# Performance work log

Hardware: AMD Instinct MI355X
Metric: run time of the kernel (lower is better)

The kernel has to match this reference:

```python
import jax, jax.numpy as jnp
from jax import lax
import numpy as np

PRE_NMS_TOPN = 2000
POST_NMS_TOPN = 300
NMS_IOU_THRESHOLD = 0.7
EPS = 1e-8


def setup_inputs() -> dict:
    key = jax.random.key(0)
    k1, k2 = jax.random.split(key, 2)
    B, H, W, A = 64, 100, 100, 9
    # small-magnitude deltas so exp(dh/dw) stays sane, as real RPN outputs do
    rpn_bbox_deltas = jax.random.normal(k1, (B, H, W, A * 4), dtype=jnp.float32) * 0.1
    rpn_labels = jax.random.uniform(k2, (B, H, W, A), dtype=jnp.float32)
    # grid anchors, normalized coords, 3 scales x 3 ratios = 9 per position
    ys = (jnp.arange(H, dtype=jnp.float32) + 0.5) / H
    xs = (jnp.arange(W, dtype=jnp.float32) + 0.5) / W
    scales = jnp.array([0.1, 0.2, 0.4], dtype=jnp.float32)
    ratios = jnp.array([0.5, 1.0, 2.0], dtype=jnp.float32)
    hh = (scales[:, None] * jnp.sqrt(ratios)[None, :]).reshape(-1)  # [9]
    ww = (scales[:, None] / jnp.sqrt(ratios)[None, :]).reshape(-1)  # [9]
    cy, cx = jnp.meshgrid(ys, xs, indexing="ij")  # [H,W]
    cy, cx = cy[..., None], cx[..., None]         # [H,W,1]
    anchors = jnp.stack(
        [cy - hh / 2, cx - ww / 2, cy + hh / 2, cx + ww / 2], axis=-1
    ).reshape(-1, 4)  # [H*W*9, 4] = [90000, 4]
    return {"rpn_bbox_deltas": rpn_bbox_deltas, "rpn_labels": rpn_labels, "anchors": anchors}


def _decode_deltas(anchors, deltas):
    # anchors [N,4] (y1,x1,y2,x2), deltas [B,N,4] (dy,dx,dh,dw)
    anc_h = anchors[:, 2] - anchors[:, 0]
    anc_w = anchors[:, 3] - anchors[:, 1]
    anc_cy = anchors[:, 0] + 0.5 * anc_h
    anc_cx = anchors[:, 1] + 0.5 * anc_w
    h = jnp.exp(deltas[..., 2]) * anc_h
    w = jnp.exp(deltas[..., 3]) * anc_w
    cy = deltas[..., 0] * anc_h + anc_cy
    cx = deltas[..., 1] * anc_w + anc_cx
    y1 = cy - 0.5 * h
    x1 = cx - 0.5 * w
    return jnp.stack([y1, x1, y1 + h, x1 + w], axis=-1)  # [B,N,4]


def _nms_single(boxes):
    # boxes [PRE,4] already sorted by score descending; greedy hard NMS
    n = boxes.shape[0]
    area = jnp.maximum(boxes[:, 2] - boxes[:, 0], 0.0) * jnp.maximum(boxes[:, 3] - boxes[:, 1], 0.0)
    idx = jnp.arange(n)

    def body(i, keep):
        b = boxes[i]
        yy1 = jnp.maximum(b[0], boxes[:, 0])
        xx1 = jnp.maximum(b[1], boxes[:, 1])
        yy2 = jnp.minimum(b[2], boxes[:, 2])
        xx2 = jnp.minimum(b[3], boxes[:, 3])
        inter = jnp.maximum(yy2 - yy1, 0.0) * jnp.maximum(xx2 - xx1, 0.0)
        iou = inter / (area[i] + area - inter + EPS)
        suppress = (iou > NMS_IOU_THRESHOLD) & (idx > i) & keep[i]
        return keep & ~suppress

    keep = lax.fori_loop(0, n, body, jnp.ones((n,), dtype=bool))
    # compact kept boxes (score order) into fixed [POST,4], zero-padded
    pos = jnp.where(keep, jnp.cumsum(keep) - 1, POST_NMS_TOPN)
    pos = jnp.minimum(pos, POST_NMS_TOPN)
    out = jnp.zeros((POST_NMS_TOPN + 1, 4), dtype=boxes.dtype).at[pos].set(boxes)[:POST_NMS_TOPN]
    return jnp.clip(out, 0.0, 1.0)  # clip_boxes=True in tf combined NMS


def reference(rpn_bbox_deltas, rpn_labels, anchors):
    B = rpn_bbox_deltas.shape[0]
    N = anchors.shape[0]
    deltas = rpn_bbox_deltas.reshape(B, N, 4)
    labels = rpn_labels.reshape(B, N)
    boxes = _decode_deltas(anchors, deltas)             # [B,N,4]
    _, pre_idx = lax.top_k(labels, PRE_NMS_TOPN)        # [B,PRE] sorted desc
    pre_boxes = jnp.take_along_axis(boxes, pre_idx[..., None], axis=1)  # [B,PRE,4]
    roi_bboxes = jax.vmap(_nms_single)(pre_boxes)       # [B,POST,4]
    return lax.stop_gradient(roi_bboxes)
```

## Files before the change

kernel.cpp:

```cpp
#include <hip/hip_runtime.h>
#include <stdint.h>


#define PRE 2000
#define POST 300
#define TILE 512
#define IOU_THR 0.7f
#define EPSV 1e-8f
#define SORTN 2048
#define NBINS 2048
#define DESTCAP 4096
#define CANDCAP 512
#define CONS 1984
#define SL 16
#define KBUF 768

typedef unsigned long long u64;

__device__ __forceinline__ uint32_t flip_f32(uint32_t b) {
    return b ^ ((uint32_t)((int32_t)b >> 31) | 0x80000000u);
}

__device__ __forceinline__ int bin_of(float s) {
    int bn = (int)(s * 2048.0f);
    return min(max(bn, 0), NBINS - 1);
}

__device__ __forceinline__ u64 make_key(float s, int idx, int bn) {
    uint32_t ub = flip_f32(__float_as_uint(s));
    return ((u64)ub << 32) | ((uint32_t)bn << 20) |
           (uint32_t)(0xFFFFF - idx);
}

__device__ __forceinline__ bool iou_gt(const float4& bi, float ai,
                                       const float4& bj, float aj) {
    float yy1 = fmaxf(bi.x, bj.x);
    float xx1 = fmaxf(bi.y, bj.y);
    float yy2 = fminf(bi.z, bj.z);
    float xx2 = fminf(bi.w, bj.w);
    float inter = fmaxf(yy2 - yy1, 0.f) * fmaxf(xx2 - xx1, 0.f);
    float iou = inter / (ai + aj - inter + EPSV);
    return iou > IOU_THR;
}

__device__ __forceinline__ float area_of(const float4& bx) {
    return fmaxf(bx.z - bx.x, 0.f) * fmaxf(bx.w - bx.y, 0.f);
}

__device__ __forceinline__ u64 cs_keep(u64 v, u64 pv, int i, int j, int k) {
    bool lower   = ((i & j) == 0);
    bool desc    = ((i & k) == 0);
    bool keepmax = (desc == lower);
    u64 mx = v > pv ? v : pv;
    u64 mn = v > pv ? pv : v;
    return keepmax ? mx : mn;
}

__global__ __launch_bounds__(256) void k1_gather(
    const float4* __restrict__ score4,
    u64* __restrict__ g_pairs,
    int* __restrict__ g_scnt,
    int N)
{
    const int blk = blockIdx.x;
    const int b   = blk / SL;
    const int s   = blk % SL;
    const int tid = threadIdx.x;
    const int F4PB = N >> 2;
    const int F4PS = (F4PB + SL - 1) / SL;

    __shared__ u64 keybuf[KBUF];
    __shared__ int kcnt;

    if (tid == 0) kcnt = 0;
    __syncthreads();

    const float4* src = score4 + (size_t)b * F4PB;
    const int n0 = s * F4PS, n1 = min(n0 + F4PS, F4PB);
    for (int n = n0 + tid; n < n1; n += 256) {
        float4 v = src[n];
        float sv[4] = {v.x, v.y, v.z, v.w};
#pragma unroll
        for (int c = 0; c < 4; ++c) {
            int bn = bin_of(sv[c]);
            if (bn >= CONS) {
                int q = atomicAdd(&kcnt, 1);
                if (q < KBUF) keybuf[q] = make_key(sv[c], 4 * n + c, bn);
            }
        }
    }
    __syncthreads();

    if (tid == 0) g_scnt[b * SL + s] = kcnt;
    int lc = min(kcnt, KBUF);
    u64* gp = g_pairs + ((size_t)b * SL + s) * KBUF;
    for (int i = tid; i < lc; i += 256) gp[i] = keybuf[i];
}

__global__ __launch_bounds__(1024) void k2_sort(
    const float4* __restrict__ score4,
    const u64*  __restrict__ g_pairs,
    const int*  __restrict__ g_scnt,
    const float4* __restrict__ deltas,
    const float4* __restrict__ anchors,
    float4* __restrict__ g_boxes,
    float*  __restrict__ g_area,
    uint32_t* __restrict__ g_supT,
    int N)
{
    const int b    = blockIdx.x;
    const int tid  = threadIdx.x;
    const int lane = tid & 63;
    const int wv   = tid >> 6;

    __shared__ u64 dest[DESTCAP];
    __shared__ float4 sbox[TILE];
    __shared__ u64 cand[CANDCAP];
    __shared__ uint32_t hist64[64];
    __shared__ int segbase64[64];
    __shared__ uint32_t cur64[64];
    __shared__ int scnt_s[SL];
    __shared__ uint32_t wtot[16];
    __shared__ int sh_flag, sh_total, sh_bsel, sh_tprime, sh_cnt, sh_nc;
    __shared__ uint32_t sh_pivot;

    const int F4PB = N >> 2;

    if (tid < SL) scnt_s[tid] = g_scnt[b * SL + tid];
    if (tid < 64) { hist64[tid] = 0u; cur64[tid] = 0u; }
    if (tid == 0) { sh_flag = 0; sh_cnt = 0; sh_nc = 0; }
    __syncthreads();

    {
        int raw = scnt_s[wv];
        if (raw > KBUF) sh_flag = 1;
        int cs = min(raw, KBUF);
        const u64* gp = g_pairs + ((size_t)b * SL + wv) * KBUF;
        for (int i = lane; i < cs; i += 64) {
            int b64 = (int)((gp[i] >> 20) & 0xFFFu) - CONS;
            atomicAdd(&hist64[b64], 1u);
        }
    }
    __syncthreads();

    if (wv == 0) {
        int h = (int)hist64[lane];
        int ssum = h;
#pragma unroll
        for (int off = 1; off < 64; off <<= 1) {
            int t = __shfl_down(ssum, off, 64);
            if (lane + off < 64) ssum += t;
        }
        segbase64[lane] = ssum - h;
        if (lane == 0) sh_total = ssum;
        if (h > 128) sh_flag = 1;
    }
    __syncthreads();
    const int total = sh_total;
    if (tid == 0 && (total < PRE || total > DESTCAP)) sh_flag = 1;
    __syncthreads();
    const bool flag = (sh_flag != 0);

    if (!flag) {
        int cs = min(scnt_s[wv], KBUF);
        const u64* gp = g_pairs + ((size_t)b * SL + wv) * KBUF;
        for (int i = lane; i < cs; i += 64) {
            u64 key = gp[i];
            int b64 = (int)((key >> 20) & 0xFFFu) - CONS;
            int c = (int)atomicAdd(&cur64[b64], 1u);
            dest[segbase64[b64] + c] = key;
        }
        __syncthreads();
        for (int sgi = wv; sgi < 64; sgi += 16) {
            int n = (int)cur64[sgi];
            if (n <= 0) continue;
            int base = segbase64[sgi];
            if (n <= 64) {
                u64 e = (lane < n) ? dest[base + lane] : 0ull;
#pragma unroll
                for (int k = 2; k <= 64; k <<= 1)
                    for (int j = k >> 1; j > 0; j >>= 1)
                        e = cs_keep(e, __shfl_xor(e, j, 64), lane, j, k);
                if (lane < n) dest[base + lane] = e;
            } else {
                u64 e0 = (lane < n) ? dest[base + lane] : 0ull;
                u64 e1 = (lane + 64 < n) ? dest[base + lane + 64] : 0ull;
#pragma unroll
                for (int k = 2; k <= 128; k <<= 1) {
                    for (int j = k >> 1; j > 0; j >>= 1) {
                        if (j == 64) {
                            u64 a = e0, c = e1;
                            e0 = cs_keep(a, c, lane, 64, k);
                            e1 = cs_keep(c, a, lane + 64, 64, k);
                        } else {
                            e0 = cs_keep(e0, __shfl_xor(e0, j, 64), lane, j, k);
                            e1 = cs_keep(e1, __shfl_xor(e1, j, 64), lane + 64, j, k);
                        }
                    }
                }
                if (lane < n) dest[base + lane] = e0;
                if (lane + 64 < n) dest[base + lane + 64] = e1;
            }
        }
        __syncthreads();
    } else {
        uint32_t* hist = (uint32_t*)sbox;
        hist[tid] = 0u; hist[tid + 1024] = 0u;
        if (tid == 0) { sh_cnt = 0; sh_nc = 0; }
        __syncthreads();
        const float4* src = score4 + (size_t)b * F4PB;
        for (int n = tid; n < F4PB; n += 1024) {
            float4 v = src[n];
            atomicAdd(&hist[bin_of(v.x)], 1u);
            atomicAdd(&hist[bin_of(v.y)], 1u);
            atomicAdd(&hist[bin_of(v.z)], 1u);
            atomicAdd(&hist[bin_of(v.w)], 1u);
        }
        __syncthreads();
        {
            const int i0 = wv * 128 + lane;
            const int i1 = i0 + 64;
            int h0 = (int)hist[i0];
            int h1 = (int)hist[i1];
            int s0 = h0, s1 = h1;
#pragma unroll
            for (int off = 1; off < 64; off <<= 1) {
                int t0 = __shfl_down(s0, off, 64);
                int t1 = __shfl_down(s1, off, 64);
                if (lane + off < 64) { s0 += t0; s1 += t1; }
            }
            int sum_h1 = __shfl(s1, 0, 64);
            if (lane == 0) wtot[wv] = (uint32_t)(__shfl(s0, 0, 64) + sum_h1);
            __syncthreads();
            int offtot = 0;
            for (int w2 = wv + 1; w2 < 16; ++w2) offtot += (int)wtot[w2];
            int S0 = s0 + sum_h1 + offtot;
            int S1 = s1 + offtot;
            if (S0 >= PRE && S0 - h0 < PRE) { sh_bsel = i0; sh_tprime = PRE - (S0 - h0); }
            if (S1 >= PRE && S1 - h1 < PRE) { sh_bsel = i1; sh_tprime = PRE - (S1 - h1); }
        }
        __syncthreads();
        const int bsel   = sh_bsel;
        const int tprime = sh_tprime;
        __syncthreads();
        for (int n = tid; n < F4PB; n += 1024) {
            float4 v = src[n];
            float sv[4] = {v.x, v.y, v.z, v.w};
#pragma unroll
            for (int c = 0; c < 4; ++c) {
                int bn = bin_of(sv[c]);
                if (bn >= bsel) {
                    u64 key = make_key(sv[c], 4 * n + c, bn);
                    if (bn > bsel) {
                        int q = atomicAdd(&sh_cnt, 1);
                        if (q < SORTN) dest[q] = key;
                    } else {
                        int t = atomicAdd(&sh_nc, 1);
                        if (t < CANDCAP) cand[t] = key;
                    }
                }
            }
        }
        __syncthreads();
        const int nc = min(sh_nc, CANDCAP);
        for (int i = tid; i < nc; i += 1024) {
            uint32_t vi = (uint32_t)(cand[i] >> 32);
            int g = 0, e = 0;
            for (int j = 0; j < nc; ++j) {
                uint32_t vj = (uint32_t)(cand[j] >> 32);
                g += (vj > vi);
                e += (vj == vi);
            }
            if (g < tprime && g + e >= tprime) sh_pivot = vi;
        }
        __syncthreads();
        const uint32_t pivot = sh_pivot;
        for (int i = tid; i < nc; i += 1024) {
            uint32_t vi = (uint32_t)(cand[i] >> 32);
            if (vi >= pivot) {
                int q = atomicAdd(&sh_cnt, 1);
                if (q < SORTN) dest[q] = cand[i];
            }
        }
        __syncthreads();
        const int tt = min(sh_cnt, SORTN);
        for (int q = tt + tid; q < SORTN; q += 1024) dest[q] = 0ull;
        __syncthreads();
        {
            const int i0 = wv * 128 + lane;
            const int i1 = i0 + 64;
            u64 e0 = dest[i0];
            u64 e1 = dest[i1];
            for (int k = 2; k <= SORTN; k <<= 1) {
                for (int j = k >> 1; j > 0; j >>= 1) {
                    if (j >= 128) {
                        dest[i0] = e0;
                        dest[i1] = e1;
                        __syncthreads();
                        u64 p0 = dest[i0 ^ j];
                        u64 p1 = dest[i1 ^ j];
                        __syncthreads();
                        e0 = cs_keep(e0, p0, i0, j, k);
                        e1 = cs_keep(e1, p1, i1, j, k);
                    } else if (j == 64) {
                        u64 a = e0, c = e1;
                        e0 = cs_keep(a, c, i0, 64, k);
                        e1 = cs_keep(c, a, i1, 64, k);
                    } else {
                        e0 = cs_keep(e0, __shfl_xor(e0, j, 64), i0, j, k);
                        e1 = cs_keep(e1, __shfl_xor(e1, j, 64), i1, j, k);
                    }
                }
            }
            dest[i0] = e0;
            dest[i1] = e1;
        }
        __syncthreads();
    }

    const float4* dl = deltas + (size_t)b * N;
    for (int r = tid; r < PRE; r += 1024) {
        u64 key = dest[r];
        uint32_t idx = 0xFFFFFu - (uint32_t)(key & 0xFFFFFull);
        float4 bx = make_float4(0.f, 0.f, 0.f, 0.f);
        float  ar = 0.f;
        if (idx < (uint32_t)N) {
            float4 d  = dl[idx];
            float4 an = anchors[idx];
            float ah  = an.z - an.x;
            float aw  = an.w - an.y;
            float acy = an.x + 0.5f * ah;
            float acx = an.y + 0.5f * aw;
            float h   = expf(d.z) * ah;
            float w   = expf(d.w) * aw;
            float cy  = d.x * ah + acy;
            float cx  = d.y * aw + acx;
            float y1  = cy - 0.5f * h;
            float x1  = cx - 0.5f * w;
            bx = make_float4(y1, x1, y1 + h, x1 + w);
            ar = fmaxf(bx.z - bx.x, 0.f) * fmaxf(bx.w - bx.y, 0.f);
        }
        g_boxes[(size_t)b * PRE + r] = bx;
        g_area [(size_t)b * PRE + r] = ar;
        if (r < TILE) sbox[r] = bx;
    }
    __syncthreads();

    {
        int q  = tid >> 7;
        int j  = (tid >> 1) & 63;
        int w2 = tid & 1;
        int C  = q * 64 + j;
        float4 bc = sbox[C];
        float  ac = area_of(bc);
        uint32_t bits = 0u;
#pragma unroll
        for (int c = 0; c < 32; ++c) {
            int R = q * 64 + w2 * 32 + c;
            float4 br = sbox[R];
            float  ar = area_of(br);
            bool gt = (R < C) & iou_gt(br, ar, bc, ac);
            bits |= ((uint32_t)gt) << c;
        }
        g_supT[((size_t)b * TILE + C) * 2 + w2] = bits;
    }
}

__global__ __launch_bounds__(256) void k4_supmat(
    const float4* __restrict__ g_boxes,
    uint32_t* __restrict__ g_supmat)
{
    const int b   = blockIdx.x >> 4;
    const int s   = blockIdx.x & 15;
    const int tid = threadIdx.x;

    __shared__ float4 box[TILE];
    for (int i = tid; i < TILE; i += 256)
        box[i] = g_boxes[(size_t)b * PRE + i];
    __syncthreads();

    const int rbase = s * 32;
#pragma unroll
    for (int k = 0; k < 2; ++k) {
        int idx = tid + k * 256;
        int row = rbase + (idx & 31);
        int w   = idx >> 5;
        int jbase = w << 5;
        float4 bi = box[row];
        float  ai = area_of(bi);
        uint32_t bits = 0u;
        if (jbase + 31 > row) {
#pragma unroll
            for (int c = 0; c < 32; ++c) {
                int j = jbase + c;
                float4 bj = box[j];
                float  aj = area_of(bj);
                bool gt = (j > row) & iou_gt(bi, ai, bj, aj);
                bits |= ((uint32_t)gt) << c;
            }
        }
        g_supmat[((size_t)b * TILE + row) * 16 + w] = bits;
    }
}

__global__ __launch_bounds__(64) void k5_sweep(
    const uint32_t* __restrict__ g_supmat,
    const u64*    __restrict__ g_supT64,
    const float4* __restrict__ g_boxes,
    const float*  __restrict__ g_area,
    float4* __restrict__ out)
{
    const int b    = blockIdx.x;
    const int lane = threadIdx.x;

    __shared__ uint32_t kept[POST];
    __shared__ u64 sh_keepbits[TILE / 64];
    __shared__ uint32_t fmask[(PRE - TILE + 31) / 32];
    __shared__ int sh_kc;

    const u64* tdbase = g_supT64 + (size_t)b * TILE;

    uint32_t removedw = 0u;
    int kc = 0, nq = 0;
    u64 cw_cur = tdbase[lane];
    for (int q = 0; q < TILE / 64; ++q) {
        u64 cw_next = (q < TILE / 64 - 1) ? tdbase[(q + 1) * 64 + lane] : 0ull;
        const int cbase = q << 6;
        uint32_t rlo = (uint32_t)__builtin_amdgcn_readlane((int)removedw, 2 * q);
        uint32_t rhi = (uint32_t)__builtin_amdgcn_readlane((int)removedw, 2 * q + 1);
        u64 avail = ~(((u64)rhi << 32) | rlo);
        u64 K = 0ull;
        while (avail) {
            int i = __ffsll((long long)avail) - 1;
            K |= (1ull << i);
            u64 supp = __ballot(((cw_cur >> i) & 1ull) != 0ull);
            avail &= ~(supp | (1ull << i));
        }
        if (lane == 0) sh_keepbits[q] = K;
        kc += __popcll(K);
        nq = q + 1;
        if (kc >= POST) break;
        if (K) {
            const int w = lane & 15;
            const int g = lane >> 4;
            const uint32_t* gs =
                g_supmat + ((size_t)b * TILE + cbase + g * 16) * 16 + w;
            uint32_t acc = 0u;
#pragma unroll
            for (int r = 0; r < 16; ++r)
                if ((K >> (g * 16 + r)) & 1ull) acc |= gs[(size_t)r * 16];
            acc |= (uint32_t)__shfl_xor((int)acc, 16, 64);
            acc |= (uint32_t)__shfl_xor((int)acc, 32, 64);
            if (lane < 16) removedw |= acc;
        }
        cw_cur = cw_next;
    }
    {
        int base = 0;
        for (int q = 0; q < nq; ++q) {
            u64 kbq = sh_keepbits[q];
            int pos = base + __popcll(kbq & ((1ull << lane) - 1));
            if (((kbq >> lane) & 1ull) && pos < POST)
                kept[pos] = (uint32_t)(q * 64 + lane);
            base += __popcll(kbq);
        }
        if (lane == 0) sh_kc = min(kc, POST);
    }
    __syncthreads();
    int kcf = sh_kc;

    if (kcf < POST) {
        for (int w = lane; w < (PRE - TILE + 31) / 32; w += 64) fmask[w] = 0u;
        __syncthreads();
        for (int j = TILE + lane; j < PRE; j += 64) {
            float4 bj = g_boxes[(size_t)b * PRE + j];
            float  aj = g_area [(size_t)b * PRE + j];
            bool supd = false;
            for (int k = 0; k < kcf; ++k) {
                int i = (int)kept[k];
                float4 bi = g_boxes[(size_t)b * PRE + i];
                float  ai = g_area [(size_t)b * PRE + i];
                if (iou_gt(bi, ai, bj, aj)) { supd = true; break; }
            }
            if (supd) atomicOr(&fmask[(j - TILE) >> 5], 1u << ((j - TILE) & 31));
        }
        __syncthreads();
        int i = TILE;
        while (i < PRE && kcf < POST) {
            while (i < PRE && ((fmask[(i - TILE) >> 5] >> ((i - TILE) & 31)) & 1u)) ++i;
            if (i >= PRE) break;
            if (lane == 0) kept[kcf] = (uint32_t)i;
            ++kcf;
            if (kcf >= POST) break;
            float4 bi = g_boxes[(size_t)b * PRE + i];
            float  ai = g_area [(size_t)b * PRE + i];
            for (int j = i + 1 + lane; j < PRE; j += 64) {
                float4 bj = g_boxes[(size_t)b * PRE + j];
                float  aj = g_area [(size_t)b * PRE + j];
                if (iou_gt(bi, ai, bj, aj))
                    atomicOr(&fmask[(j - TILE) >> 5], 1u << ((j - TILE) & 31));
            }
            ++i;
            __syncthreads();
        }
    }
    __syncthreads();

    float4* ob = out + (size_t)b * POST;
    for (int r = lane; r < POST; r += 64) {
        float4 o = make_float4(0.f, 0.f, 0.f, 0.f);
        if (r < kcf) {
            float4 bx = g_boxes[(size_t)b * PRE + kept[r]];
            o.x = fminf(fmaxf(bx.x, 0.f), 1.f);
            o.y = fminf(fmaxf(bx.y, 0.f), 1.f);
            o.z = fminf(fmaxf(bx.z, 0.f), 1.f);
            o.w = fminf(fmaxf(bx.w, 0.f), 1.f);
        }
        ob[r] = o;
    }
}

extern "C" void kernel_launch(void* const* d_in, const int* in_sizes, int n_in,
                              void* d_out, int out_size, void* d_ws, size_t ws_size,
                              hipStream_t stream) {
    const float4* deltas  = (const float4*)d_in[0];
    const float*  labels  = (const float*)d_in[1];
    const float4* anchors = (const float4*)d_in[2];
    const float4* score4  = (const float4*)labels;
    float4*       outp    = (float4*)d_out;
    const int N = in_sizes[2] / 4;
    const int B = in_sizes[1] / N;

    char* ws = (char*)d_ws;
    const size_t SZ_BOXES  = (size_t)B * PRE * 16;
    const size_t SZ_PAIRS  = (size_t)B * SL * KBUF * 8;
    const size_t SZ_SUPMAT = (size_t)B * TILE * 16 * 4;
    const size_t SZ_SUPT   = (size_t)B * TILE * 8;
    const size_t SZ_AREA   = (size_t)B * PRE * 4;
    float4*   g_boxes  = (float4*)ws;
    u64*      g_pairs  = (u64*)(ws + SZ_BOXES);
    uint32_t* g_supmat = (uint32_t*)(ws + SZ_BOXES + SZ_PAIRS);
    uint32_t* g_supT   = (uint32_t*)(ws + SZ_BOXES + SZ_PAIRS + SZ_SUPMAT);
    float*    g_area   = (float*)(ws + SZ_BOXES + SZ_PAIRS + SZ_SUPMAT + SZ_SUPT);
    int*      g_scnt   = (int*)(ws + SZ_BOXES + SZ_PAIRS + SZ_SUPMAT + SZ_SUPT + SZ_AREA);

    k1_gather<<<B * SL, 256, 0, stream>>>(score4, g_pairs, g_scnt, N);
    k2_sort<<<B, 1024, 0, stream>>>(score4, g_pairs, g_scnt, deltas, anchors,
                                    g_boxes, g_area, g_supT, N);
    k4_supmat<<<B * 16, 256, 0, stream>>>(g_boxes, g_supmat);
    k5_sweep<<<B, 64, 0, stream>>>(g_supmat, (const u64*)g_supT,
                                   g_boxes, g_area, outp);
}
```

Measured before the change: 88.40 us.

## Split box decode out of sort kernel and move supT build into supmat kernel

The sort kernel no longer decodes boxes or builds the transposed suppression tiles. It writes the sorted keys to a new global buffer, and a separate decode kernel with four blocks per image gathers deltas and anchors and writes boxes and areas. The supT computation moves into the supmat kernel's first eight blocks, and the sweep's conditional loads become branchless masked ORs. This spreads the serial per-image tail across more blocks, at the cost of an extra launch and a global round-trip for the sorted keys.

```diff
diff --git a/kernel.cpp b/kernel.cpp
--- a/kernel.cpp
+++ b/kernel.cpp
@@ -101,11 +101,7 @@
     const float4* __restrict__ score4,
     const u64*  __restrict__ g_pairs,
     const int*  __restrict__ g_scnt,
-    const float4* __restrict__ deltas,
-    const float4* __restrict__ anchors,
-    float4* __restrict__ g_boxes,
-    float*  __restrict__ g_area,
-    uint32_t* __restrict__ g_supT,
+    u64* __restrict__ g_sorted,
     int N)
 {
     const int b    = blockIdx.x;
@@ -114,7 +110,7 @@
     const int wv   = tid >> 6;
 
     __shared__ u64 dest[DESTCAP];
-    __shared__ float4 sbox[TILE];
+    __shared__ uint32_t hist2048[NBINS];
     __shared__ u64 cand[CANDCAP];
     __shared__ uint32_t hist64[64];
     __shared__ int segbase64[64];
@@ -203,25 +199,26 @@
             }
         }
         __syncthreads();
+        g_sorted[(size_t)b * SORTN + tid]        = dest[tid];
+        g_sorted[(size_t)b * SORTN + tid + 1024] = dest[tid + 1024];
     } else {
-        uint32_t* hist = (uint32_t*)sbox;
-        hist[tid] = 0u; hist[tid + 1024] = 0u;
+        hist2048[tid] = 0u; hist2048[tid + 1024] = 0u;
         if (tid == 0) { sh_cnt = 0; sh_nc = 0; }
         __syncthreads();
         const float4* src = score4 + (size_t)b * F4PB;
         for (int n = tid; n < F4PB; n += 1024) {
             float4 v = src[n];
-            atomicAdd(&hist[bin_of(v.x)], 1u);
-            atomicAdd(&hist[bin_of(v.y)], 1u);
-            atomicAdd(&hist[bin_of(v.z)], 1u);
-            atomicAdd(&hist[bin_of(v.w)], 1u);
+            atomicAdd(&hist2048[bin_of(v.x)], 1u);
+            atomicAdd(&hist2048[bin_of(v.y)], 1u);
+            atomicAdd(&hist2048[bin_of(v.z)], 1u);
+            atomicAdd(&hist2048[bin_of(v.w)], 1u);
         }
         __syncthreads();
         {
             const int i0 = wv * 128 + lane;
             const int i1 = i0 + 64;
-            int h0 = (int)hist[i0];
-            int h1 = (int)hist[i1];
+            int h0 = (int)hist2048[i0];
+            int h1 = (int)hist2048[i1];
             int s0 = h0, s1 = h1;
 #pragma unroll
             for (int off = 1; off < 64; off <<= 1) {
@@ -242,7 +239,6 @@
         __syncthreads();
         const int bsel   = sh_bsel;
         const int tprime = sh_tprime;
-        __syncthreads();
         for (int n = tid; n < F4PB; n += 1024) {
             float4 v = src[n];
             float sv[4] = {v.x, v.y, v.z, v.w};
@@ -312,15 +308,28 @@
                     }
                 }
             }
-            dest[i0] = e0;
-            dest[i1] = e1;
-        }
-        __syncthreads();
-    }
+            g_sorted[(size_t)b * SORTN + i0] = e0;
+            g_sorted[(size_t)b * SORTN + i1] = e1;
+        }
+    }
+}
+
+__global__ __launch_bounds__(256) void k3_decode(
+    const float4* __restrict__ deltas,
+    const float4* __restrict__ anchors,
+    const u64*  __restrict__ g_sorted,
+    float4* __restrict__ g_boxes,
+    float*  __restrict__ g_area,
+    int N)
+{
+    const int b   = blockIdx.x >> 2;
+    const int s   = blockIdx.x & 3;
+    const int tid = threadIdx.x;
+    const int r0 = s * 512, r1 = min(r0 + 512, PRE);
 
     const float4* dl = deltas + (size_t)b * N;
-    for (int r = tid; r < PRE; r += 1024) {
-        u64 key = dest[r];
+    for (int r = r0 + tid; r < r1; r += 256) {
+        u64 key = g_sorted[(size_t)b * SORTN + r];
         uint32_t idx = 0xFFFFFu - (uint32_t)(key & 0xFFFFFull);
         float4 bx = make_float4(0.f, 0.f, 0.f, 0.f);
         float  ar = 0.f;
@@ -342,33 +351,13 @@
         }
         g_boxes[(size_t)b * PRE + r] = bx;
         g_area [(size_t)b * PRE + r] = ar;
-        if (r < TILE) sbox[r] = bx;
-    }
-    __syncthreads();
-
-    {
-        int q  = tid >> 7;
-        int j  = (tid >> 1) & 63;
-        int w2 = tid & 1;
-        int C  = q * 64 + j;
-        float4 bc = sbox[C];
-        float  ac = area_of(bc);
-        uint32_t bits = 0u;
-#pragma unroll
-        for (int c = 0; c < 32; ++c) {
-            int R = q * 64 + w2 * 32 + c;
-            float4 br = sbox[R];
-            float  ar = area_of(br);
-            bool gt = (R < C) & iou_gt(br, ar, bc, ac);
-            bits |= ((uint32_t)gt) << c;
-        }
-        g_supT[((size_t)b * TILE + C) * 2 + w2] = bits;
     }
 }
 
 __global__ __launch_bounds__(256) void k4_supmat(
     const float4* __restrict__ g_boxes,
-    uint32_t* __restrict__ g_supmat)
+    uint32_t* __restrict__ g_supmat,
+    uint32_t* __restrict__ g_supT)
 {
     const int b   = blockIdx.x >> 4;
     const int s   = blockIdx.x & 15;
@@ -400,6 +389,25 @@
             }
         }
         g_supmat[((size_t)b * TILE + row) * 16 + w] = bits;
+    }
+
+    if (s < 8 && tid < 128) {
+        int q  = s;
+        int j  = tid >> 1;
+        int w2 = tid & 1;
+        int C  = q * 64 + j;
+        float4 bc = box[C];
+        float  ac = area_of(bc);
+        uint32_t bits = 0u;
+#pragma unroll
+        for (int c = 0; c < 32; ++c) {
+            int R = q * 64 + w2 * 32 + c;
+            float4 br = box[R];
+            float  ar = area_of(br);
+            bool gt = (R < C) & iou_gt(br, ar, bc, ac);
+            bits |= ((uint32_t)gt) << c;
+        }
+        g_supT[((size_t)b * TILE + C) * 2 + w2] = bits;
     }
 }
 
@@ -447,8 +455,11 @@
                 g_supmat + ((size_t)b * TILE + cbase + g * 16) * 16 + w;
             uint32_t acc = 0u;
 #pragma unroll
-            for (int r = 0; r < 16; ++r)
-                if ((K >> (g * 16 + r)) & 1ull) acc |= gs[(size_t)r * 16];
+            for (int r = 0; r < 16; ++r) {
+                uint32_t v = gs[(size_t)r * 16];
+                uint32_t m = (uint32_t)0 - (uint32_t)((K >> (g * 16 + r)) & 1ull);
+                acc |= (v & m);
+            }
             acc |= (uint32_t)__shfl_xor((int)acc, 16, 64);
             acc |= (uint32_t)__shfl_xor((int)acc, 32, 64);
             if (lane < 16) removedw |= acc;
@@ -534,20 +545,23 @@
     char* ws = (char*)d_ws;
     const size_t SZ_BOXES  = (size_t)B * PRE * 16;
     const size_t SZ_PAIRS  = (size_t)B * SL * KBUF * 8;
+    const size_t SZ_SORTED = (size_t)B * SORTN * 8;
     const size_t SZ_SUPMAT = (size_t)B * TILE * 16 * 4;
     const size_t SZ_SUPT   = (size_t)B * TILE * 8;
     const size_t SZ_AREA   = (size_t)B * PRE * 4;
     float4*   g_boxes  = (float4*)ws;
     u64*      g_pairs  = (u64*)(ws + SZ_BOXES);
-    uint32_t* g_supmat = (uint32_t*)(ws + SZ_BOXES + SZ_PAIRS);
-    uint32_t* g_supT   = (uint32_t*)(ws + SZ_BOXES + SZ_PAIRS + SZ_SUPMAT);
-    float*    g_area   = (float*)(ws + SZ_BOXES + SZ_PAIRS + SZ_SUPMAT + SZ_SUPT);
-    int*      g_scnt   = (int*)(ws + SZ_BOXES + SZ_PAIRS + SZ_SUPMAT + SZ_SUPT + SZ_AREA);
+    u64*      g_sorted = (u64*)(ws + SZ_BOXES + SZ_PAIRS);
+    uint32_t* g_supmat = (uint32_t*)(ws + SZ_BOXES + SZ_PAIRS + SZ_SORTED);
+    uint32_t* g_supT   = (uint32_t*)(ws + SZ_BOXES + SZ_PAIRS + SZ_SORTED + SZ_SUPMAT);
+    float*    g_area   = (float*)(ws + SZ_BOXES + SZ_PAIRS + SZ_SORTED + SZ_SUPMAT + SZ_SUPT);
+    int*      g_scnt   = (int*)(ws + SZ_BOXES + SZ_PAIRS + SZ_SORTED + SZ_SUPMAT + SZ_SUPT + SZ_AREA);
 
     k1_gather<<<B * SL, 256, 0, stream>>>(score4, g_pairs, g_scnt, N);
-    k2_sort<<<B, 1024, 0, stream>>>(score4, g_pairs, g_scnt, deltas, anchors,
-                                    g_boxes, g_area, g_supT, N);
-    k4_supmat<<<B * 16, 256, 0, stream>>>(g_boxes, g_supmat);
+    k2_sort<<<B, 1024, 0, stream>>>(score4, g_pairs, g_scnt, g_sorted, N);
+    k3_decode<<<B * 4, 256, 0, stream>>>(deltas, anchors, g_sorted,
+                                         g_boxes, g_area, N);
+    k4_supmat<<<B * 16, 256, 0, stream>>>(g_boxes, g_supmat, g_supT);
     k5_sweep<<<B, 64, 0, stream>>>(g_supmat, (const u64*)g_supT,
                                    g_boxes, g_area, outp);
 }
```

Result: faster. 80.90 us (-8.5%).
